# Kernel optimization log

Hardware: AMD Instinct MI355X
Metric: run time of the kernel (lower is better)

Reference implementation:

```python
import jax, jax.numpy as jnp
import numpy as np

NUM_HEADS = 16
ROPE_THETA = 10000.0


def _rope_cos_sin(T, head_dim, dtype):
    # inv_freq over even indices; cos/sin shape [T, head_dim//2]
    inv_freq = 1.0 / (ROPE_THETA ** (jnp.arange(0, head_dim, 2, dtype=jnp.float32) / head_dim))
    t = jnp.arange(T, dtype=jnp.float32)
    freqs = jnp.outer(t, inv_freq)  # [T, hd/2]
    return jnp.cos(freqs).astype(dtype), jnp.sin(freqs).astype(dtype)


def _apply_rope(x, cos, sin):
    # x: [B,H,T,hd]; de-interleave even/odd, rotate, concat halves
    x1 = x[..., ::2]
    x2 = x[..., 1::2]
    return jnp.concatenate([x1 * cos - x2 * sin, x1 * sin + x2 * cos], axis=-1)


def setup_inputs() -> dict:
    key = jax.random.key(0)
    k1, k2, k3 = jax.random.split(key, 3)
    B, T, C = 2, 2048, 2048
    x = jax.random.normal(k1, (B, T, C), dtype=jnp.float32)
    w_qkv = jax.random.normal(k2, (3 * C, C), dtype=jnp.float32) * (C ** -0.5)
    w_proj = jax.random.normal(k3, (C, C), dtype=jnp.float32) * (C ** -0.5)
    causal_mask = jnp.tril(jnp.ones((T, T), dtype=bool))[None, None, :, :]  # [1,1,T,T]
    return {"x": x, "w_qkv": w_qkv, "w_proj": w_proj, "causal_mask": causal_mask}


def reference(x, w_qkv, w_proj, causal_mask):
    B, T, C = x.shape
    H = NUM_HEADS
    hd = C // H
    scale = hd ** -0.5

    qkv = jnp.einsum('btc,oc->bto', x, w_qkv)  # [B,T,3C]
    qkv = qkv.reshape(B, T, 3, H, hd).transpose(2, 0, 3, 1, 4)  # [3,B,H,T,hd]
    q, k, v = qkv[0], qkv[1], qkv[2]

    cos, sin = _rope_cos_sin(T, hd, x.dtype)
    q = _apply_rope(q, cos, sin)
    k = _apply_rope(k, cos, sin)

    scores = jnp.einsum('bhqd,bhkd->bhqk', q, k) * scale  # [B,H,T,T]
    scores = jnp.where(causal_mask, scores, -jnp.inf)
    attn = jax.nn.softmax(scores, axis=-1)
    out = jnp.einsum('bhqk,bhkd->bhqd', attn, v)  # [B,H,T,hd]
    out = out.transpose(0, 2, 1, 3).reshape(B, T, C)
    return jnp.einsum('btc,oc->bto', out, w_proj)
```

## Files before the change

kernel.cpp:

```cpp
#include <hip/hip_runtime.h>
#include <stdint.h>

typedef float f32x4 __attribute__((ext_vector_type(4)));
typedef __bf16 bf16x8 __attribute__((ext_vector_type(8)));
typedef unsigned short u16x8 __attribute__((ext_vector_type(8)));

__device__ __forceinline__ unsigned short f2bf(float f) {
  union { float f; unsigned u; } x; x.f = f;
  unsigned r = x.u + 0x7fffu + ((x.u >> 16) & 1u);
  return (unsigned short)(r >> 16);
}
__device__ __forceinline__ float bf2f(unsigned short u) {
  union { unsigned u; float f; } x; x.u = ((unsigned)u) << 16;
  return x.f;
}
__device__ __forceinline__ void async_copy16(void* lds, const void* g) {
  __builtin_amdgcn_global_load_lds(
      (const unsigned int __attribute__((address_space(1)))*)g,
      (unsigned int __attribute__((address_space(3)))*)lds, 16, 0, 0);
}
__device__ __forceinline__ f32x4 mfma16(bf16x8 a, bf16x8 b, f32x4 c) {
  return __builtin_amdgcn_mfma_f32_16x16x32_bf16(a, b, c, 0, 0, 0);
}

__global__ __launch_bounds__(256) void cvt_f32_bf16(
    const float* __restrict__ in, unsigned short* __restrict__ out, int n8) {
  int stride = gridDim.x * blockDim.x;
  for (int i = blockIdx.x * blockDim.x + threadIdx.x; i < n8; i += stride) {
    const float4* p = (const float4*)in + (size_t)i * 2;
    float4 a = p[0], b = p[1];
    u16x8 o;
    o[0] = f2bf(a.x); o[1] = f2bf(a.y); o[2] = f2bf(a.z); o[3] = f2bf(a.w);
    o[4] = f2bf(b.x); o[5] = f2bf(b.y); o[6] = f2bf(b.z); o[7] = f2bf(b.w);
    *((u16x8*)out + i) = o;
  }
}

__global__ __launch_bounds__(256) void rope_table(float2* __restrict__ cs) {
  int idx = blockIdx.x * 256 + threadIdx.x;
  if (idx >= 2048 * 64) return;
  int t = idx >> 6, j = idx & 63;
  float inv = expf(-0.14391156516026f * (float)j);
  float ang = (float)t * inv;
  cs[idx] = make_float2(cosf(ang), sinf(ang));
}

template <bool OUT_F32>
__global__ __launch_bounds__(512, 2) void gemm_bt2(
    const unsigned short* __restrict__ A, const unsigned short* __restrict__ Bt,
    void* __restrict__ Cout, int M, int N, int K) {
  __shared__ unsigned short sA[3][128 * 32];
  __shared__ unsigned short sB[3][256 * 32];
  const int tid = threadIdx.x;
  const int w = tid >> 6, l = tid & 63;
  const int wm = w >> 2, wn = w & 3;
  const int g = l >> 4, lr = l & 15;
  const int m0 = blockIdx.y * 128, n0 = blockIdx.x * 256;

  f32x4 acc[4][4];
#pragma unroll
  for (int i = 0; i < 4; ++i)
#pragma unroll
    for (int j = 0; j < 4; ++j) acc[i][j] = f32x4{0.f, 0.f, 0.f, 0.f};

  auto stage = [&](int buf, int kt) {
    const int k0 = kt * 32;
    {
      int unit = w * 64 + l;
      int row = unit >> 2, s = unit & 3;
      int sg = s ^ (row & 3) ^ ((row >> 2) & 3);
      async_copy16(&sA[buf][w * 512],
                   A + (size_t)(m0 + row) * K + k0 + sg * 8);
    }
#pragma unroll
    for (int j = 0; j < 2; ++j) {
      int unit = j * 512 + w * 64 + l;
      int row = unit >> 2, s = unit & 3;
      int sg = s ^ (row & 3) ^ ((row >> 2) & 3);
      async_copy16(&sB[buf][(j * 8 + w) * 512],
                   Bt + (size_t)(n0 + row) * K + k0 + sg * 8);
    }
  };

  const int NK = K / 32;
  stage(0, 0);
  stage(1, 1);
  for (int kt = 0; kt < NK; ++kt) {
    const int cur = kt % 3;
    if (kt + 1 < NK) asm volatile("s_waitcnt vmcnt(3)" ::: "memory");
    else             asm volatile("s_waitcnt vmcnt(0)" ::: "memory");
    __syncthreads();
    if (kt + 2 < NK) stage((kt + 2) % 3, kt + 2);

    bf16x8 af[4], bq[4];
#pragma unroll
    for (int mi = 0; mi < 4; ++mi) {
      int row = wm * 64 + mi * 16 + lr;
      int sl = g ^ (row & 3) ^ ((row >> 2) & 3);
      af[mi] = *(const bf16x8*)&sA[cur][row * 32 + sl * 8];
    }
#pragma unroll
    for (int ni = 0; ni < 4; ++ni) {
      int row = wn * 64 + ni * 16 + lr;
      int sl = g ^ (row & 3) ^ ((row >> 2) & 3);
      bq[ni] = *(const bf16x8*)&sB[cur][row * 32 + sl * 8];
    }
    __builtin_amdgcn_s_setprio(1);
#pragma unroll
    for (int mi = 0; mi < 4; ++mi)
#pragma unroll
      for (int ni = 0; ni < 4; ++ni)
        acc[mi][ni] = mfma16(af[mi], bq[ni], acc[mi][ni]);
    __builtin_amdgcn_s_setprio(0);
    __syncthreads();
  }

#pragma unroll
  for (int mi = 0; mi < 4; ++mi)
#pragma unroll
    for (int ni = 0; ni < 4; ++ni) {
      int col = n0 + wn * 64 + ni * 16 + lr;
#pragma unroll
      for (int jr = 0; jr < 4; ++jr) {
        int row = m0 + wm * 64 + mi * 16 + g * 4 + jr;
        float v = acc[mi][ni][jr];
        if (OUT_F32)
          ((float*)Cout)[(size_t)row * N + col] = v;
        else
          ((unsigned short*)Cout)[(size_t)row * N + col] = f2bf(v);
      }
    }
}

__global__ __launch_bounds__(256) void prep_rope(
    const unsigned short* __restrict__ qkv, const float2* __restrict__ cs,
    unsigned short* __restrict__ Q, unsigned short* __restrict__ K,
    unsigned short* __restrict__ Vt) {
  const int tt = blockIdx.x, h = blockIdx.y, b = blockIdx.z;
  const int t0 = tt * 64;
  const int tid = threadIdx.x;
  __shared__ unsigned short vt[64][130];

#pragma unroll 4
  for (int i = 0; i < 32; ++i) {
    int lin = i * 256 + tid;
    int r = lin >> 7, j = lin & 127;
    int t = t0 + r;
    int jj = j & 63;
    size_t rowbase = ((size_t)(b * 2048 + t)) * 6144 + h * 128;
    float2 c_s = cs[t * 64 + jj];
    float q1 = bf2f(qkv[rowbase + 2 * jj]);
    float q2 = bf2f(qkv[rowbase + 2 * jj + 1]);
    float k1 = bf2f(qkv[rowbase + 2048 + 2 * jj]);
    float k2 = bf2f(qkv[rowbase + 2048 + 2 * jj + 1]);
    float qo = (j < 64) ? (q1 * c_s.x - q2 * c_s.y) : (q1 * c_s.y + q2 * c_s.x);
    float ko = (j < 64) ? (k1 * c_s.x - k2 * c_s.y) : (k1 * c_s.y + k2 * c_s.x);
    size_t obase = ((size_t)((b * 16 + h) * 2048 + t)) * 128 + j;
    Q[obase] = f2bf(qo);
    K[obase] = f2bf(ko);
    vt[r][j] = qkv[rowbase + 4096 + j];
  }
  __syncthreads();
  size_t vbase = ((size_t)((b * 16 + h) * 128)) * 2048 + t0;
#pragma unroll 4
  for (int i = 0; i < 32; ++i) {
    int lin = i * 256 + tid;
    int d = lin >> 6, c = lin & 63;
    Vt[vbase + (size_t)d * 2048 + c] = vt[c][d];
  }
}

__global__ __launch_bounds__(512, 2) void attn_fwd(
    const unsigned short* __restrict__ Q, const unsigned short* __restrict__ K,
    const unsigned short* __restrict__ Vt, unsigned short* __restrict__ AO) {
  const int bid = blockIdx.x;
  const int bh = (bid & 7) * 4 + ((bid >> 3) & 3);
  const int qp = bid >> 5;
  const int b = bh >> 4, h = bh & 15;
  __shared__ unsigned short sK[2][64 * 128];
  __shared__ unsigned short sV[2][128 * 64];
  __shared__ unsigned short sP[8][16 * 64];
  const int tid = threadIdx.x, w = tid >> 6, l = tid & 63;
  const int g = l >> 4, lr = l & 15;
  const size_t qkbase = (size_t)bh * 2048 * 128;
  const size_t vbase = (size_t)bh * 128 * 2048;
  const float scale = 0.08838834764831845f;

  auto stage = [&](int buf, int kt) {
#pragma unroll
    for (int j = 0; j < 2; ++j) {
      int r = w * 2 + j;
      int kv = r * 4 + (l >> 4);
      int sc = (l & 15) ^ (kv & 15);
      async_copy16(&sK[buf][r * 512],
                   K + qkbase + (size_t)(kt * 64 + kv) * 128 + sc * 8);
      int d = r * 8 + (l >> 3);
      int sv = (l & 7) ^ (d & 7);
      async_copy16(&sV[buf][r * 512],
                   Vt + vbase + (size_t)d * 2048 + kt * 64 + sv * 8);
    }
  };

  auto process = [&](int qt) {
    const int q0w = qt * 128 + w * 16;
    bf16x8 qf[4];
#pragma unroll
    for (int kc = 0; kc < 4; ++kc)
      qf[kc] = *(const bf16x8*)(Q + qkbase + (size_t)(q0w + lr) * 128 +
                                kc * 32 + g * 8);
    f32x4 of[8];
    float mrow[4], lsum[4];
#pragma unroll
    for (int nd = 0; nd < 8; ++nd) of[nd] = f32x4{0.f, 0.f, 0.f, 0.f};
#pragma unroll
    for (int jr = 0; jr < 4; ++jr) { mrow[jr] = -1e30f; lsum[jr] = 0.f; }

    const int NT = 2 * qt + 2;
    __syncthreads();
    stage(0, 0);
    int cur = 0;
    for (int kt = 0; kt < NT; ++kt) {
      asm volatile("s_waitcnt vmcnt(0)" ::: "memory");
      __syncthreads();
      if (kt + 1 < NT) stage(cur ^ 1, kt + 1);

      if (kt * 64 <= q0w + 15) {
        f32x4 sacc[4];
#pragma unroll
        for (int ni = 0; ni < 4; ++ni) sacc[ni] = f32x4{0.f, 0.f, 0.f, 0.f};
#pragma unroll
        for (int kc = 0; kc < 4; ++kc)
#pragma unroll
          for (int ni = 0; ni < 4; ++ni) {
            int kv = ni * 16 + lr;
            bf16x8 kf = *(const bf16x8*)&sK[cur][kv * 128 +
                          (((kc * 4 + g) ^ (kv & 15)) << 3)];
            sacc[ni] = mfma16(qf[kc], kf, sacc[ni]);
          }

        const bool needmask = (kt * 64 + 63 > q0w);
        float pm[4] = {-1e30f, -1e30f, -1e30f, -1e30f};
#pragma unroll
        for (int ni = 0; ni < 4; ++ni)
#pragma unroll
          for (int jr = 0; jr < 4; ++jr) {
            float sv = sacc[ni][jr] * scale;
            if (needmask) {
              int kvg = kt * 64 + ni * 16 + lr;
              int qg = q0w + g * 4 + jr;
              if (kvg > qg) sv = -1e30f;
            }
            sacc[ni][jr] = sv;
            pm[jr] = fmaxf(pm[jr], sv);
          }
#pragma unroll
        for (int jr = 0; jr < 4; ++jr) {
          float v = pm[jr];
          v = fmaxf(v, __shfl_xor(v, 1));
          v = fmaxf(v, __shfl_xor(v, 2));
          v = fmaxf(v, __shfl_xor(v, 4));
          v = fmaxf(v, __shfl_xor(v, 8));
          float mnew = fmaxf(mrow[jr], v);
          float fac = __expf(mrow[jr] - mnew);
          mrow[jr] = mnew;
          float rsum = 0.f;
#pragma unroll
          for (int ni = 0; ni < 4; ++ni) {
            float p = __expf(sacc[ni][jr] - mnew);
            sacc[ni][jr] = p;
            rsum += p;
          }
          rsum += __shfl_xor(rsum, 1);
          rsum += __shfl_xor(rsum, 2);
          rsum += __shfl_xor(rsum, 4);
          rsum += __shfl_xor(rsum, 8);
          lsum[jr] = lsum[jr] * fac + rsum;
#pragma unroll
          for (int nd = 0; nd < 8; ++nd) of[nd][jr] *= fac;
        }

#pragma unroll
        for (int ni = 0; ni < 4; ++ni)
#pragma unroll
          for (int jr = 0; jr < 4; ++jr) {
            int q = g * 4 + jr;
            int kv = ni * 16 + lr;
            sP[w][q * 64 + (((kv >> 3) ^ (q & 7)) << 3) + (kv & 7)] =
                f2bf(sacc[ni][jr]);
          }

#pragma unroll
        for (int kc = 0; kc < 2; ++kc) {
          bf16x8 pa = *(const bf16x8*)&sP[w][lr * 64 +
                        (((kc * 4 + g) ^ (lr & 7)) << 3)];
#pragma unroll
          for (int nd = 0; nd < 8; ++nd) {
            int d = nd * 16 + lr;
            bf16x8 vb = *(const bf16x8*)&sV[cur][d * 64 +
                          (((kc * 4 + g) ^ (d & 7)) << 3)];
            of[nd] = mfma16(pa, vb, of[nd]);
          }
        }
      }
      cur ^= 1;
    }

#pragma unroll
    for (int nd = 0; nd < 8; ++nd)
#pragma unroll
      for (int jr = 0; jr < 4; ++jr) {
        int qrow = q0w + g * 4 + jr;
        int d = nd * 16 + lr;
        AO[(size_t)(b * 2048 + qrow) * 2048 + h * 128 + d] =
            f2bf(of[nd][jr] / lsum[jr]);
      }
  };

  process(qp);
  process(15 - qp);
}

extern "C" void kernel_launch(void* const* d_in, const int* in_sizes, int n_in,
                              void* d_out, int out_size, void* d_ws, size_t ws_size,
                              hipStream_t stream) {
  (void)in_sizes; (void)n_in; (void)out_size; (void)ws_size;
  const float* x = (const float*)d_in[0];
  const float* wqkv = (const float*)d_in[1];
  const float* wproj = (const float*)d_in[2];

  char* ws = (char*)d_ws;
  unsigned short* WPROJB = (unsigned short*)(ws + 0);
  unsigned short* XB     = (unsigned short*)(ws + 8388608);
  unsigned short* WQKVB  = (unsigned short*)(ws + 25165824);
  unsigned short* QKV    = (unsigned short*)(ws + 50331648);
  unsigned short* Kr     = (unsigned short*)(ws + 100663296);
  unsigned short* Vt     = (unsigned short*)(ws + 117440512);
  float2*         CS     = (float2*)(ws + 134217728);
  unsigned short* AO = XB;
  unsigned short* Qr = WQKVB;

  rope_table<<<512, 256, 0, stream>>>(CS);
  cvt_f32_bf16<<<2048, 256, 0, stream>>>(x, XB, 8388608 / 8);
  cvt_f32_bf16<<<2048, 256, 0, stream>>>(wqkv, WQKVB, 12582912 / 8);
  cvt_f32_bf16<<<1024, 256, 0, stream>>>(wproj, WPROJB, 4194304 / 8);
  gemm_bt2<false><<<dim3(24, 32), 512, 0, stream>>>(XB, WQKVB, QKV, 4096, 6144, 2048);
  prep_rope<<<dim3(32, 16, 2), 256, 0, stream>>>(QKV, CS, Qr, Kr, Vt);
  attn_fwd<<<256, 512, 0, stream>>>(Qr, Kr, Vt, AO);
  gemm_bt2<true><<<dim3(8, 32), 512, 0, stream>>>(AO, WPROJB, d_out, 4096, 2048, 2048);
}
```

Before: 464.2 us.

## Restructure GEMM into ping-pong halves with split staging and XCD-aware block mapping

```diff
diff --git a/kernel.cpp b/kernel.cpp
--- a/kernel.cpp
+++ b/kernel.cpp
@@ -45,84 +45,121 @@
   cs[idx] = make_float2(cosf(ang), sinf(ang));
 }
 
-template <bool OUT_F32>
-__global__ __launch_bounds__(512, 2) void gemm_bt2(
+template <int TBM, bool OUT_F32>
+__global__ __launch_bounds__(512, 2) void gemm8p(
     const unsigned short* __restrict__ A, const unsigned short* __restrict__ Bt,
-    void* __restrict__ Cout, int M, int N, int K) {
-  __shared__ unsigned short sA[3][128 * 32];
+    void* __restrict__ Cout, int M, int N, int K, int ntx) {
+  constexpr int MF = TBM / 32;
+  constexpr int AL = TBM / 128;
+  constexpr int L = AL + 2;
+  __shared__ unsigned short sA[3][TBM * 32];
   __shared__ unsigned short sB[3][256 * 32];
   const int tid = threadIdx.x;
   const int w = tid >> 6, l = tid & 63;
   const int wm = w >> 2, wn = w & 3;
   const int g = l >> 4, lr = l & 15;
-  const int m0 = blockIdx.y * 128, n0 = blockIdx.x * 256;
-
-  f32x4 acc[4][4];
-#pragma unroll
-  for (int i = 0; i < 4; ++i)
+  const int bid = (int)blockIdx.x;
+  const int chunk = (int)gridDim.x >> 3;
+  const int sid = (bid & 7) * chunk + (bid >> 3);
+  const int by = sid / ntx, bx = sid - by * ntx;
+  const int m0 = by * TBM, n0 = bx * 256;
+
+  f32x4 acc[MF][4];
+#pragma unroll
+  for (int i = 0; i < MF; ++i)
 #pragma unroll
     for (int j = 0; j < 4; ++j) acc[i][j] = f32x4{0.f, 0.f, 0.f, 0.f};
 
-  auto stage = [&](int buf, int kt) {
+  auto stageA = [&](int buf, int kt) {
     const int k0 = kt * 32;
-    {
-      int unit = w * 64 + l;
-      int row = unit >> 2, s = unit & 3;
-      int sg = s ^ (row & 3) ^ ((row >> 2) & 3);
-      async_copy16(&sA[buf][w * 512],
+#pragma unroll
+    for (int i = 0; i < AL; ++i) {
+      int u = i * 512 + w * 64 + l;
+      int row = u >> 2, s = u & 3;
+      int sg = s ^ ((row & 3) ^ ((row >> 2) & 3));
+      async_copy16(&sA[buf][(i * 512 + w * 64) * 8],
                    A + (size_t)(m0 + row) * K + k0 + sg * 8);
     }
-#pragma unroll
-    for (int j = 0; j < 2; ++j) {
-      int unit = j * 512 + w * 64 + l;
-      int row = unit >> 2, s = unit & 3;
-      int sg = s ^ (row & 3) ^ ((row >> 2) & 3);
-      async_copy16(&sB[buf][(j * 8 + w) * 512],
+  };
+  auto stageB = [&](int buf, int kt) {
+    const int k0 = kt * 32;
+#pragma unroll
+    for (int i = 0; i < 2; ++i) {
+      int u = i * 512 + w * 64 + l;
+      int row = u >> 2, s = u & 3;
+      int sg = s ^ ((row & 3) ^ ((row >> 2) & 3));
+      async_copy16(&sB[buf][(i * 512 + w * 64) * 8],
                    Bt + (size_t)(n0 + row) * K + k0 + sg * 8);
     }
   };
 
   const int NK = K / 32;
-  stage(0, 0);
-  stage(1, 1);
+  stageA(0, 0); stageB(0, 0);
+  stageA(1, 1); stageB(1, 1);
+
   for (int kt = 0; kt < NK; ++kt) {
     const int cur = kt % 3;
-    if (kt + 1 < NK) asm volatile("s_waitcnt vmcnt(3)" ::: "memory");
-    else             asm volatile("s_waitcnt vmcnt(0)" ::: "memory");
-    __syncthreads();
-    if (kt + 2 < NK) stage((kt + 2) % 3, kt + 2);
-
-    bf16x8 af[4], bq[4];
-#pragma unroll
-    for (int mi = 0; mi < 4; ++mi) {
-      int row = wm * 64 + mi * 16 + lr;
-      int sl = g ^ (row & 3) ^ ((row >> 2) & 3);
-      af[mi] = *(const bf16x8*)&sA[cur][row * 32 + sl * 8];
-    }
+    const int nxt = (kt + 2) % 3;
+    if (kt + 1 < NK) {
+      if constexpr (L == 4) asm volatile("s_waitcnt vmcnt(4)" ::: "memory");
+      else                  asm volatile("s_waitcnt vmcnt(3)" ::: "memory");
+    } else {
+      asm volatile("s_waitcnt vmcnt(0)" ::: "memory");
+    }
+    __builtin_amdgcn_s_barrier();
+
+    bf16x8 bq[4];
 #pragma unroll
     for (int ni = 0; ni < 4; ++ni) {
       int row = wn * 64 + ni * 16 + lr;
-      int sl = g ^ (row & 3) ^ ((row >> 2) & 3);
+      int sl = g ^ ((row & 3) ^ ((row >> 2) & 3));
       bq[ni] = *(const bf16x8*)&sB[cur][row * 32 + sl * 8];
     }
+    bf16x8 afA[MF / 2];
+#pragma unroll
+    for (int mi = 0; mi < MF / 2; ++mi) {
+      int row = wm * (TBM / 2) + mi * 16 + lr;
+      int sl = g ^ ((row & 3) ^ ((row >> 2) & 3));
+      afA[mi] = *(const bf16x8*)&sA[cur][row * 32 + sl * 8];
+    }
+    if (kt + 2 < NK) stageA(nxt, kt + 2);
+    __builtin_amdgcn_s_barrier();
     __builtin_amdgcn_s_setprio(1);
 #pragma unroll
-    for (int mi = 0; mi < 4; ++mi)
+    for (int mi = 0; mi < MF / 2; ++mi)
 #pragma unroll
       for (int ni = 0; ni < 4; ++ni)
-        acc[mi][ni] = mfma16(af[mi], bq[ni], acc[mi][ni]);
+        acc[mi][ni] = mfma16(afA[mi], bq[ni], acc[mi][ni]);
     __builtin_amdgcn_s_setprio(0);
-    __syncthreads();
+    __builtin_amdgcn_s_barrier();
+
+    bf16x8 afB[MF / 2];
+#pragma unroll
+    for (int mi = 0; mi < MF / 2; ++mi) {
+      int row = wm * (TBM / 2) + (MF / 2 + mi) * 16 + lr;
+      int sl = g ^ ((row & 3) ^ ((row >> 2) & 3));
+      afB[mi] = *(const bf16x8*)&sA[cur][row * 32 + sl * 8];
+    }
+    if (kt + 2 < NK) stageB(nxt, kt + 2);
+    __builtin_amdgcn_s_barrier();
+    __builtin_amdgcn_s_setprio(1);
+#pragma unroll
+    for (int mi = 0; mi < MF / 2; ++mi)
+#pragma unroll
+      for (int ni = 0; ni < 4; ++ni)
+        acc[MF / 2 + mi][ni] = mfma16(afB[mi], bq[ni], acc[MF / 2 + mi][ni]);
+    __builtin_amdgcn_s_setprio(0);
+    __builtin_amdgcn_s_barrier();
   }
 
 #pragma unroll
-  for (int mi = 0; mi < 4; ++mi)
+  for (int mi = 0; mi < MF; ++mi)
 #pragma unroll
     for (int ni = 0; ni < 4; ++ni) {
       int col = n0 + wn * 64 + ni * 16 + lr;
 #pragma unroll
       for (int jr = 0; jr < 4; ++jr) {
-        int row = m0 + wm * 64 + mi * 16 + g * 4 + jr;
+        int row = m0 + wm * (TBM / 2) + mi * 16 + g * 4 + jr;
         float v = acc[mi][ni][jr];
         if (OUT_F32)
           ((float*)Cout)[(size_t)row * N + col] = v;
@@ -343,8 +380,8 @@
   cvt_f32_bf16<<<2048, 256, 0, stream>>>(x, XB, 8388608 / 8);
   cvt_f32_bf16<<<2048, 256, 0, stream>>>(wqkv, WQKVB, 12582912 / 8);
   cvt_f32_bf16<<<1024, 256, 0, stream>>>(wproj, WPROJB, 4194304 / 8);
-  gemm_bt2<false><<<dim3(24, 32), 512, 0, stream>>>(XB, WQKVB, QKV, 4096, 6144, 2048);
+  gemm8p<256, false><<<384, 512, 0, stream>>>(XB, WQKVB, QKV, 4096, 6144, 2048, 24);
   prep_rope<<<dim3(32, 16, 2), 256, 0, stream>>>(QKV, CS, Qr, Kr, Vt);
   attn_fwd<<<256, 512, 0, stream>>>(Qr, Kr, Vt, AO);
-  gemm_bt2<true><<<dim3(8, 32), 512, 0, stream>>>(AO, WPROJB, d_out, 4096, 2048, 2048);
-}
+  gemm8p<128, true><<<256, 512, 0, stream>>>(AO, WPROJB, d_out, 4096, 2048, 2048, 8);
+}
```

Result: no change. 458.2 us (-1.3%).

## Double GEMM K-tile to 64 and split main loop into two interleaved phases

Applied to the files above, without the earlier changes.

```diff
diff --git a/kernel.cpp b/kernel.cpp
--- a/kernel.cpp
+++ b/kernel.cpp
@@ -46,11 +46,11 @@
 }
 
 template <bool OUT_F32>
-__global__ __launch_bounds__(512, 2) void gemm_bt2(
+__global__ __launch_bounds__(512, 2) void gemm_dp(
     const unsigned short* __restrict__ A, const unsigned short* __restrict__ Bt,
     void* __restrict__ Cout, int M, int N, int K) {
-  __shared__ unsigned short sA[3][128 * 32];
-  __shared__ unsigned short sB[3][256 * 32];
+  __shared__ unsigned short sA[3][128 * 64];
+  __shared__ unsigned short sB[3][256 * 64];
   const int tid = threadIdx.x;
   const int w = tid >> 6, l = tid & 63;
   const int wm = w >> 2, wn = w & 3;
@@ -63,56 +63,86 @@
 #pragma unroll
     for (int j = 0; j < 4; ++j) acc[i][j] = f32x4{0.f, 0.f, 0.f, 0.f};
 
-  auto stage = [&](int buf, int kt) {
-    const int k0 = kt * 32;
-    {
-      int unit = w * 64 + l;
-      int row = unit >> 2, s = unit & 3;
-      int sg = s ^ (row & 3) ^ ((row >> 2) & 3);
-      async_copy16(&sA[buf][w * 512],
-                   A + (size_t)(m0 + row) * K + k0 + sg * 8);
-    }
-#pragma unroll
-    for (int j = 0; j < 2; ++j) {
-      int unit = j * 512 + w * 64 + l;
-      int row = unit >> 2, s = unit & 3;
-      int sg = s ^ (row & 3) ^ ((row >> 2) & 3);
-      async_copy16(&sB[buf][(j * 8 + w) * 512],
-                   Bt + (size_t)(n0 + row) * K + k0 + sg * 8);
+  auto stageA = [&](int buf, int kt) {
+    const int k0 = kt * 64;
+#pragma unroll
+    for (int i = 0; i < 2; ++i) {
+      int u = i * 512 + tid;
+      int row = u >> 3, sl = u & 7;
+      int sg = sl ^ (row & 7);
+      async_copy16(&sA[buf][u * 8], A + (size_t)(m0 + row) * K + k0 + sg * 8);
     }
   };
-
-  const int NK = K / 32;
-  stage(0, 0);
-  stage(1, 1);
+  auto stageB = [&](int buf, int kt, int half) {
+    const int k0 = kt * 64;
+#pragma unroll
+    for (int i = 0; i < 2; ++i) {
+      int u = (half * 2 + i) * 512 + tid;
+      int row = u >> 3, sl = u & 7;
+      int sg = sl ^ (row & 7);
+      async_copy16(&sB[buf][u * 8], Bt + (size_t)(n0 + row) * K + k0 + sg * 8);
+    }
+  };
+
+  const int NK = K / 64;
+  stageA(0, 0); stageB(0, 0, 0); stageB(0, 0, 1);
+  stageA(1, 1); stageB(1, 1, 0); stageB(1, 1, 1);
+
   for (int kt = 0; kt < NK; ++kt) {
-    const int cur = kt % 3;
-    if (kt + 1 < NK) asm volatile("s_waitcnt vmcnt(3)" ::: "memory");
+    const int cur = kt % 3, nxt = (kt + 2) % 3;
+    if (kt + 1 < NK) asm volatile("s_waitcnt vmcnt(6)" ::: "memory");
     else             asm volatile("s_waitcnt vmcnt(0)" ::: "memory");
-    __syncthreads();
-    if (kt + 2 < NK) stage((kt + 2) % 3, kt + 2);
-
-    bf16x8 af[4], bq[4];
-#pragma unroll
-    for (int mi = 0; mi < 4; ++mi) {
-      int row = wm * 64 + mi * 16 + lr;
-      int sl = g ^ (row & 3) ^ ((row >> 2) & 3);
-      af[mi] = *(const bf16x8*)&sA[cur][row * 32 + sl * 8];
-    }
+    __builtin_amdgcn_s_barrier();
+
+    bf16x8 bq[4][2], af0[2][2];
 #pragma unroll
     for (int ni = 0; ni < 4; ++ni) {
       int row = wn * 64 + ni * 16 + lr;
-      int sl = g ^ (row & 3) ^ ((row >> 2) & 3);
-      bq[ni] = *(const bf16x8*)&sB[cur][row * 32 + sl * 8];
-    }
+#pragma unroll
+      for (int kk = 0; kk < 2; ++kk)
+        bq[ni][kk] = *(const bf16x8*)&sB[cur][row * 64 +
+                       (((kk * 4 + g) ^ (row & 7)) << 3)];
+    }
+#pragma unroll
+    for (int mi = 0; mi < 2; ++mi) {
+      int row = wm * 64 + mi * 16 + lr;
+#pragma unroll
+      for (int kk = 0; kk < 2; ++kk)
+        af0[mi][kk] = *(const bf16x8*)&sA[cur][row * 64 +
+                        (((kk * 4 + g) ^ (row & 7)) << 3)];
+    }
+    if (kt + 2 < NK) { stageA(nxt, kt + 2); stageB(nxt, kt + 2, 0); }
+    __builtin_amdgcn_s_barrier();
     __builtin_amdgcn_s_setprio(1);
 #pragma unroll
-    for (int mi = 0; mi < 4; ++mi)
-#pragma unroll
-      for (int ni = 0; ni < 4; ++ni)
-        acc[mi][ni] = mfma16(af[mi], bq[ni], acc[mi][ni]);
+    for (int kk = 0; kk < 2; ++kk)
+#pragma unroll
+      for (int mi = 0; mi < 2; ++mi)
+#pragma unroll
+        for (int ni = 0; ni < 4; ++ni)
+          acc[mi][ni] = mfma16(af0[mi][kk], bq[ni][kk], acc[mi][ni]);
     __builtin_amdgcn_s_setprio(0);
-    __syncthreads();
+
+    bf16x8 af1[2][2];
+#pragma unroll
+    for (int mi = 0; mi < 2; ++mi) {
+      int row = wm * 64 + (2 + mi) * 16 + lr;
+#pragma unroll
+      for (int kk = 0; kk < 2; ++kk)
+        af1[mi][kk] = *(const bf16x8*)&sA[cur][row * 64 +
+                        (((kk * 4 + g) ^ (row & 7)) << 3)];
+    }
+    if (kt + 2 < NK) stageB(nxt, kt + 2, 1);
+    __builtin_amdgcn_s_barrier();
+    __builtin_amdgcn_s_setprio(1);
+#pragma unroll
+    for (int kk = 0; kk < 2; ++kk)
+#pragma unroll
+      for (int mi = 0; mi < 2; ++mi)
+#pragma unroll
+        for (int ni = 0; ni < 4; ++ni)
+          acc[2 + mi][ni] = mfma16(af1[mi][kk], bq[ni][kk], acc[2 + mi][ni]);
+    __builtin_amdgcn_s_setprio(0);
   }
 
 #pragma unroll
@@ -343,8 +373,8 @@
   cvt_f32_bf16<<<2048, 256, 0, stream>>>(x, XB, 8388608 / 8);
   cvt_f32_bf16<<<2048, 256, 0, stream>>>(wqkv, WQKVB, 12582912 / 8);
   cvt_f32_bf16<<<1024, 256, 0, stream>>>(wproj, WPROJB, 4194304 / 8);
-  gemm_bt2<false><<<dim3(24, 32), 512, 0, stream>>>(XB, WQKVB, QKV, 4096, 6144, 2048);
+  gemm_dp<false><<<dim3(24, 32), 512, 0, stream>>>(XB, WQKVB, QKV, 4096, 6144, 2048);
   prep_rope<<<dim3(32, 16, 2), 256, 0, stream>>>(QKV, CS, Qr, Kr, Vt);
   attn_fwd<<<256, 512, 0, stream>>>(Qr, Kr, Vt, AO);
-  gemm_bt2<true><<<dim3(8, 32), 512, 0, stream>>>(AO, WPROJB, d_out, 4096, 2048, 2048);
-}
+  gemm_dp<true><<<dim3(8, 32), 512, 0, stream>>>(AO, WPROJB, d_out, 4096, 2048, 2048);
+}
```

After: 423.6 us. 8.7% less time.
